# Performance work log

Hardware: AMD Instinct MI355X
Metric: run time of the kernel (lower is better)

The kernel has to match this reference:

```python
import jax, jax.numpy as jnp
import numpy as np

D_MODEL = 2048
NUM_HEADS = 16
D_K = D_MODEL // NUM_HEADS
THETA = 10000.0
BATCH, SEQ = 2, 2048


def setup_inputs() -> dict:
    key = jax.random.key(0)
    ks = jax.random.split(key, 5)
    scale = 1.0 / np.sqrt(D_MODEL)
    x = jax.random.normal(ks[0], (BATCH, SEQ, D_MODEL), dtype=jnp.float32)
    token_positions = jnp.broadcast_to(jnp.arange(SEQ, dtype=jnp.int32)[None, :], (BATCH, SEQ))
    Wq = jax.random.normal(ks[1], (D_MODEL, D_MODEL), dtype=jnp.float32) * scale
    Wk = jax.random.normal(ks[2], (D_MODEL, D_MODEL), dtype=jnp.float32) * scale
    Wv = jax.random.normal(ks[3], (D_MODEL, D_MODEL), dtype=jnp.float32) * scale
    Wo = jax.random.normal(ks[4], (D_MODEL, D_MODEL), dtype=jnp.float32) * scale
    return {"x": x, "token_positions": token_positions, "Wq": Wq, "Wk": Wk, "Wv": Wv, "Wo": Wo}


def _apply_rope(t, positions):
    # t: [b, h, s, d_k]; positions: [b, s]. Interleaved-pair rotation.
    half = D_K // 2
    inv_freq = THETA ** (-jnp.arange(0, half, dtype=jnp.float32) * 2.0 / D_K)  # [half]
    ang = positions.astype(jnp.float32)[:, :, None] * inv_freq[None, None, :]  # [b, s, half]
    cos = jnp.cos(ang)[:, None, :, :]  # [b, 1, s, half]
    sin = jnp.sin(ang)[:, None, :, :]
    t2 = t.reshape(*t.shape[:-1], half, 2)
    x1, x2 = t2[..., 0], t2[..., 1]
    r1 = x1 * cos - x2 * sin
    r2 = x1 * sin + x2 * cos
    return jnp.stack([r1, r2], axis=-1).reshape(t.shape)


def reference(x, token_positions, Wq, Wk, Wv, Wo):
    b, s, _ = x.shape
    # Linear layers compute x @ W^T (weight stored as [out, in], no bias)
    def proj(w):
        y = jnp.einsum('bsd,ed->bse', x, w)
        return y.reshape(b, s, NUM_HEADS, D_K).transpose(0, 2, 1, 3)  # b h s d
    Q, K, V = proj(Wq), proj(Wk), proj(Wv)
    Q = _apply_rope(Q, token_positions)
    K = _apply_rope(K, token_positions)
    scores = jnp.einsum('bhqd,bhkd->bhqk', Q, K) / jnp.sqrt(jnp.float32(D_K))
    causal = jnp.tril(jnp.ones((s, s), dtype=bool))
    scores = jnp.where(causal[None, None], scores, jnp.finfo(scores.dtype).min)
    attn = jax.nn.softmax(scores, axis=-1)
    out = jnp.einsum('bhqk,bhkd->bhqd', attn, V)  # b h s d
    out = out.transpose(0, 2, 1, 3).reshape(b, s, D_MODEL)
    return jnp.einsum('bse,de->bsd', out, Wo)
```

## Files before the change

kernel.cpp:

```cpp
#include <hip/hip_runtime.h>
#include <cstdint>
#include <cstddef>

#define D_MODEL 2048
#define NHEAD 16
#define DK 128
#define SEQ 2048
#define BATCH 2
#define NTOK (BATCH * SEQ)
#define NQB 32

typedef __bf16 bf16;
typedef __bf16 bf16x2 __attribute__((ext_vector_type(2)));
typedef __bf16 bf16x4 __attribute__((ext_vector_type(4)));
typedef __bf16 bf16x8 __attribute__((ext_vector_type(8)));
typedef float f32x4 __attribute__((ext_vector_type(4)));

__device__ __forceinline__ void g2lds16(const void* g, void* l) {
  __builtin_amdgcn_global_load_lds(
      (const __attribute__((address_space(1))) void*)g,
      (__attribute__((address_space(3))) void*)l, 16, 0, 0);
}

__device__ __forceinline__ void cstore(float* p, float v) { *p = v; }
__device__ __forceinline__ void cstore(bf16* p, float v) { *p = (bf16)v; }

#define BAR()                              \
  {                                        \
    asm volatile("" ::: "memory");         \
    __builtin_amdgcn_s_barrier();          \
    asm volatile("" ::: "memory");         \
  }

__global__ void k_conv5(const float* __restrict__ X, const float* __restrict__ W0,
                        const float* __restrict__ W1, const float* __restrict__ W2,
                        const float* __restrict__ W3, bf16* __restrict__ xo,
                        bf16* __restrict__ o0, bf16* __restrict__ o1,
                        bf16* __restrict__ o2, bf16* __restrict__ o3,
                        int nx4, int nw4) {
  const float* in;
  bf16* out;
  int n;
  switch (blockIdx.y) {
    case 0: in = X; out = xo; n = nx4; break;
    case 1: in = W0; out = o0; n = nw4; break;
    case 2: in = W1; out = o1; n = nw4; break;
    case 3: in = W2; out = o2; n = nw4; break;
    default: in = W3; out = o3; n = nw4;
  }
  int i = blockIdx.x * blockDim.x + threadIdx.x;
  if (i >= n) return;
  const float4 v = ((const float4*)in)[i];
  bf16x4 o = {(bf16)v.x, (bf16)v.y, (bf16)v.z, (bf16)v.w};
  ((bf16x4*)out)[i] = o;
}

__global__ __launch_bounds__(512, 1) void k_gemm8(
    const bf16* __restrict__ A, const bf16* __restrict__ B0p, const bf16* __restrict__ B1p,
    const bf16* __restrict__ B2p, bf16* __restrict__ C0, bf16* __restrict__ C1,
    bf16* __restrict__ C2, const int* __restrict__ pos, int M, int N, int K) {
  const bf16* Bp = B0p;
  bf16* Cp = C0;
  if (blockIdx.z == 1) { Bp = B1p; Cp = C1; }
  else if (blockIdx.z == 2) { Bp = B2p; Cp = C2; }
  const bool rope = (blockIdx.z < 2);

  __shared__ bf16 Ab[2][256 * 64];
  __shared__ bf16 Bb[2][256 * 64];

  const int t = threadIdx.x;
  const int wid = t >> 6, lane = t & 63;
  const int wr = wid >> 2, wc = wid & 3;
  const int lr = lane & 15, lg = lane >> 4;
  const int bm = blockIdx.y, bn = blockIdx.x;
  const size_t arow0 = (size_t)bm * 256;
  const size_t brow0 = (size_t)bn * 256;

  const int srow = wid * 8 + (lane >> 3);
  const int schunk = ((lane & 7) ^ ((lane >> 3) & 7)) * 8;

#define STG(X, row0, k0, lb, h)                                                \
  {                                                                            \
    g2lds16(&(X)[((row0) + (h)*128 + srow) * (size_t)K + (k0) + schunk],       \
            &(lb)[((h)*128 + wid * 8) * 64]);                                  \
    g2lds16(&(X)[((row0) + (h)*128 + 64 + srow) * (size_t)K + (k0) + schunk],  \
            &(lb)[((h)*128 + 64 + wid * 8) * 64]);                             \
  }
#define LDA8(lb, mh, m, kk) \
  (*(const bf16x8*)&(lb)[((mh)*128 + wr * 64 + (m)*16 + lr) * 64 + ((((kk)*4 + lg) ^ (lr & 7)) * 8)])
#define LDB8(lb, nh, n, kk) \
  (*(const bf16x8*)&(lb)[((nh)*128 + wc * 32 + (n)*16 + lr) * 64 + ((((kk)*4 + lg) ^ (lr & 7)) * 8)])

  const int T = K >> 6;

  STG(A, arow0, 0, Ab[0], 0);
  STG(A, arow0, 0, Ab[0], 1);
  STG(Bp, brow0, 0, Bb[0], 0);
  STG(Bp, brow0, 0, Bb[0], 1);
  STG(A, arow0, 64, Ab[1], 0);

  f32x4 acc[2][2][4][2] = {};

  for (int tt = 0; tt < T; ++tt) {
    const int cur = tt & 1;
    const bf16* Ac = Ab[cur];
    const bf16* Bc = Bb[cur];
    bf16* Aw = Ab[cur];
    bf16* An = Ab[cur ^ 1];
    bf16* Bn = Bb[cur ^ 1];
    const int k1 = (tt + 1) << 6;
    const int k2 = (tt + 2) << 6;
    const bool pf1 = (tt + 1 < T);
    const bool pf2 = (tt + 2 < T);

    if (tt == T - 1) {
      asm volatile("s_waitcnt vmcnt(0)" ::: "memory");
    } else {
      asm volatile("s_waitcnt vmcnt(2)" ::: "memory");
    }
    BAR();

    bf16x8 a[4][2], b0[2][2], b1[2][2];

#pragma unroll
    for (int m = 0; m < 4; ++m)
#pragma unroll
      for (int kk = 0; kk < 2; ++kk) a[m][kk] = LDA8(Ac, 0, m, kk);
#pragma unroll
    for (int n = 0; n < 2; ++n)
#pragma unroll
      for (int kk = 0; kk < 2; ++kk) b0[n][kk] = LDB8(Bc, 0, n, kk);
    if (pf1) {
      STG(A, arow0, k1, An, 1);
      STG(Bp, brow0, k1, Bn, 0);
    }
    __builtin_amdgcn_s_setprio(1);
#pragma unroll
    for (int m = 0; m < 4; ++m)
#pragma unroll
      for (int n = 0; n < 2; ++n)
#pragma unroll
        for (int kk = 0; kk < 2; ++kk)
          acc[0][0][m][n] =
              __builtin_amdgcn_mfma_f32_16x16x32_bf16(a[m][kk], b0[n][kk], acc[0][0][m][n], 0, 0, 0);
    __builtin_amdgcn_s_setprio(0);
    BAR();

#pragma unroll
    for (int n = 0; n < 2; ++n)
#pragma unroll
      for (int kk = 0; kk < 2; ++kk) b1[n][kk] = LDB8(Bc, 1, n, kk);
    if (pf1) STG(Bp, brow0, k1, Bn, 1);
    __builtin_amdgcn_s_setprio(1);
#pragma unroll
    for (int m = 0; m < 4; ++m)
#pragma unroll
      for (int n = 0; n < 2; ++n)
#pragma unroll
        for (int kk = 0; kk < 2; ++kk)
          acc[0][1][m][n] =
              __builtin_amdgcn_mfma_f32_16x16x32_bf16(a[m][kk], b1[n][kk], acc[0][1][m][n], 0, 0, 0);
    __builtin_amdgcn_s_setprio(0);

#pragma unroll
    for (int m = 0; m < 4; ++m)
#pragma unroll
      for (int kk = 0; kk < 2; ++kk) a[m][kk] = LDA8(Ac, 1, m, kk);
    if (pf2) STG(A, arow0, k2, Aw, 0);
    __builtin_amdgcn_s_setprio(1);
#pragma unroll
    for (int m = 0; m < 4; ++m)
#pragma unroll
      for (int n = 0; n < 2; ++n)
#pragma unroll
        for (int kk = 0; kk < 2; ++kk)
          acc[1][1][m][n] =
              __builtin_amdgcn_mfma_f32_16x16x32_bf16(a[m][kk], b1[n][kk], acc[1][1][m][n], 0, 0, 0);

#pragma unroll
    for (int m = 0; m < 4; ++m)
#pragma unroll
      for (int n = 0; n < 2; ++n)
#pragma unroll
        for (int kk = 0; kk < 2; ++kk)
          acc[1][0][m][n] =
              __builtin_amdgcn_mfma_f32_16x16x32_bf16(a[m][kk], b0[n][kk], acc[1][0][m][n], 0, 0, 0);
    __builtin_amdgcn_s_setprio(0);
  }

  float invf[2];
#pragma unroll
  for (int n = 0; n < 2; ++n) {
    int f = ((wc * 32 + n * 16 + lr) & 127) >> 1;
    invf[n] = exp2f((float)f * -0.20762050593121503f);
  }
#pragma unroll
  for (int mh = 0; mh < 2; ++mh)
#pragma unroll
    for (int m = 0; m < 4; ++m) {
      size_t rowb = arow0 + mh * 128 + wr * 64 + m * 16 + lg * 4;
#pragma unroll
      for (int r = 0; r < 4; ++r) {
        float p = rope ? (float)pos[rowb + r] : 0.0f;
#pragma unroll
        for (int n = 0; n < 2; ++n) {
          float sn, cs;
          if (rope) __sincosf(p * invf[n], &sn, &cs);
#pragma unroll
          for (int nh = 0; nh < 2; ++nh) {
            float v = acc[mh][nh][m][n][r];
            float vp = __shfl_xor(v, 1);
            float outv = v;
            if (rope) outv = (lr & 1) ? (v * cs + vp * sn) : (v * cs - vp * sn);
            size_t col = brow0 + nh * 128 + wc * 32 + n * 16 + lr;
            Cp[(rowb + r) * N + col] = (bf16)outv;
          }
        }
      }
    }
#undef STG
#undef LDA8
#undef LDB8
}

__global__ __launch_bounds__(512, 1) void k_gemmPV(
    const bf16* __restrict__ A, const bf16* __restrict__ Bp, bf16* __restrict__ Cp,
    int M, int N, int K) {
  const int wg = blockIdx.x;
  const int bn = wg & 7;
  const int bm = wg >> 3;

  __shared__ bf16 Ab[2][128 * 64];
  __shared__ bf16 Bb[2][256 * 64];

  const int t = threadIdx.x;
  const int wid = t >> 6, lane = t & 63;
  const int wr = wid >> 2, wc = wid & 3;
  const int lr = lane & 15, lg = lane >> 4;
  const size_t arow0 = (size_t)bm * 128;
  const size_t brow0 = (size_t)bn * 256;

  const int srow = wid * 8 + (lane >> 3);
  const int schunk = ((lane & 7) ^ ((lane >> 3) & 7)) * 8;

#define STGA(X, k0, lb, h) \
  g2lds16(&(X)[(arow0 + (h)*64 + srow) * (size_t)K + (k0) + schunk], &(lb)[((h)*64 + wid * 8) * 64]);
#define STGB(X, k0, lb, h)                                                        \
  {                                                                               \
    g2lds16(&(X)[(brow0 + (h)*128 + srow) * (size_t)K + (k0) + schunk],           \
            &(lb)[((h)*128 + wid * 8) * 64]);                                     \
    g2lds16(&(X)[(brow0 + (h)*128 + 64 + srow) * (size_t)K + (k0) + schunk],      \
            &(lb)[((h)*128 + 64 + wid * 8) * 64]);                                \
  }
#define LDA8(lb, mh, m, kk) \
  (*(const bf16x8*)&(lb)[((mh)*64 + wr * 32 + (m)*16 + lr) * 64 + ((((kk)*4 + lg) ^ (lr & 7)) * 8)])
#define LDB8(lb, nh, n, kk) \
  (*(const bf16x8*)&(lb)[((nh)*128 + wc * 32 + (n)*16 + lr) * 64 + ((((kk)*4 + lg) ^ (lr & 7)) * 8)])

  const int T = K >> 6;

  STGA(A, 0, Ab[0], 0);
  STGA(A, 0, Ab[0], 1);
  STGB(Bp, 0, Bb[0], 0);
  STGB(Bp, 0, Bb[0], 1);
  STGA(A, 64, Ab[1], 0);

  f32x4 acc[2][2][2][2] = {};

  for (int tt = 0; tt < T; ++tt) {
    const int cur = tt & 1;
    const bf16* Ac = Ab[cur];
    const bf16* Bc = Bb[cur];
    bf16* Aw = Ab[cur];
    bf16* An = Ab[cur ^ 1];
    bf16* Bn = Bb[cur ^ 1];
    const int k1 = (tt + 1) << 6;
    const int k2 = (tt + 2) << 6;
    const bool pf1 = (tt + 1 < T);
    const bool pf2 = (tt + 2 < T);

    if (tt == T - 1) {
      asm volatile("s_waitcnt vmcnt(0)" ::: "memory");
    } else {
      asm volatile("s_waitcnt vmcnt(1)" ::: "memory");
    }
    BAR();

    bf16x8 a[2][2], b[2][2];

#pragma unroll
    for (int m = 0; m < 2; ++m)
#pragma unroll
      for (int kk = 0; kk < 2; ++kk) a[m][kk] = LDA8(Ac, 0, m, kk);
#pragma unroll
    for (int n = 0; n < 2; ++n)
#pragma unroll
      for (int kk = 0; kk < 2; ++kk) b[n][kk] = LDB8(Bc, 0, n, kk);
    if (pf1) {
      STGA(A, k1, An, 1);
      STGB(Bp, k1, Bn, 0);
    }
    __builtin_amdgcn_s_setprio(1);
#pragma unroll
    for (int m = 0; m < 2; ++m)
#pragma unroll
      for (int n = 0; n < 2; ++n)
#pragma unroll
        for (int kk = 0; kk < 2; ++kk)
          acc[0][0][m][n] =
              __builtin_amdgcn_mfma_f32_16x16x32_bf16(a[m][kk], b[n][kk], acc[0][0][m][n], 0, 0, 0);
    __builtin_amdgcn_s_setprio(0);
    BAR();

#pragma unroll
    for (int n = 0; n < 2; ++n)
#pragma unroll
      for (int kk = 0; kk < 2; ++kk) b[n][kk] = LDB8(Bc, 1, n, kk);
    if (pf1) STGB(Bp, k1, Bn, 1);
    __builtin_amdgcn_s_setprio(1);
#pragma unroll
    for (int m = 0; m < 2; ++m)
#pragma unroll
      for (int n = 0; n < 2; ++n)
#pragma unroll
        for (int kk = 0; kk < 2; ++kk)
          acc[0][1][m][n] =
              __builtin_amdgcn_mfma_f32_16x16x32_bf16(a[m][kk], b[n][kk], acc[0][1][m][n], 0, 0, 0);
    __builtin_amdgcn_s_setprio(0);
    BAR();

#pragma unroll
    for (int m = 0; m < 2; ++m)
#pragma unroll
      for (int kk = 0; kk < 2; ++kk) a[m][kk] = LDA8(Ac, 1, m, kk);
    if (pf2) STGA(A, k2, Aw, 0);
    __builtin_amdgcn_s_setprio(1);
#pragma unroll
    for (int m = 0; m < 2; ++m)
#pragma unroll
      for (int n = 0; n < 2; ++n)
#pragma unroll
        for (int kk = 0; kk < 2; ++kk)
          acc[1][1][m][n] =
              __builtin_amdgcn_mfma_f32_16x16x32_bf16(a[m][kk], b[n][kk], acc[1][1][m][n], 0, 0, 0);
    __builtin_amdgcn_s_setprio(0);
    BAR();

#pragma unroll
    for (int n = 0; n < 2; ++n)
#pragma unroll
      for (int kk = 0; kk < 2; ++kk) b[n][kk] = LDB8(Bc, 0, n, kk);
    __builtin_amdgcn_s_setprio(1);
#pragma unroll
    for (int m = 0; m < 2; ++m)
#pragma unroll
      for (int n = 0; n < 2; ++n)
#pragma unroll
        for (int kk = 0; kk < 2; ++kk)
          acc[1][0][m][n] =
              __builtin_amdgcn_mfma_f32_16x16x32_bf16(a[m][kk], b[n][kk], acc[1][0][m][n], 0, 0, 0);
    __builtin_amdgcn_s_setprio(0);
  }

#pragma unroll
  for (int mh = 0; mh < 2; ++mh)
#pragma unroll
    for (int nh = 0; nh < 2; ++nh)
#pragma unroll
      for (int m = 0; m < 2; ++m) {
        size_t rowb = arow0 + mh * 64 + wr * 32 + m * 16 + lg * 4;
#pragma unroll
        for (int n = 0; n < 2; ++n) {
          size_t col = brow0 + nh * 128 + wc * 32 + n * 16 + lr;
#pragma unroll
          for (int r = 0; r < 4; ++r) Cp[(rowb + r) * N + col] = (bf16)acc[mh][nh][m][n][r];
        }
      }
#undef STGA
#undef STGB
#undef LDA8
#undef LDB8
}

__global__ __launch_bounds__(256, 4) void k_vtrans(const bf16* __restrict__ V,
                                                   bf16* __restrict__ VT) {
  const int bh = blockIdx.z;
  const int b = bh >> 4, h = bh & 15;
  const int tt64 = blockIdx.x * 64;
  const int t = threadIdx.x;
  __shared__ bf16 L[128][72];
  const int tok_l = t & 63, dc0 = t >> 6;
#pragma unroll
  for (int p = 0; p < 4; ++p) {
    int dc = dc0 * 4 + p;
    bf16x8 v = *(const bf16x8*)&V[((size_t)(b * SEQ) + tt64 + tok_l) * D_MODEL + h * DK + dc * 8];
#pragma unroll
    for (int j = 0; j < 8; ++j) L[dc * 8 + j][tok_l] = v[j];
  }
  __syncthreads();
  const int d = t >> 1, half = t & 1;
  const size_t obase = ((size_t)bh * DK + d) * SEQ + tt64;
#pragma unroll
  for (int i = 0; i < 4; ++i) {
    int g = half * 4 + i;
    *(bf16x8*)&VT[obase + g * 8] = *(const bf16x8*)&L[d][g * 8];
  }
}

template <typename OutT>
__global__ __launch_bounds__(256, 2) void k_gemm_nt(
    const bf16* __restrict__ A, const bf16* __restrict__ B0, const bf16* __restrict__ B1,
    const bf16* __restrict__ B2, OutT* __restrict__ C0, OutT* __restrict__ C1,
    OutT* __restrict__ C2, int M, int N, int K) {
  const bf16* Bp = B0;
  OutT* Cp = C0;
  if (blockIdx.z == 1) { Bp = B1; Cp = C1; }
  else if (blockIdx.z == 2) { Bp = B2; Cp = C2; }

  __shared__ bf16 As[128 * 32];
  __shared__ bf16 Bs[128 * 32];

  const int t = threadIdx.x;
  const int w = t >> 6;
  const int lane = t & 63;
  const int lr = lane & 15;
  const int lg = lane >> 4;
  const int wr = w >> 1, wc = w & 1;
  const int bm = blockIdx.y, bn = blockIdx.x;

  f32x4 acc[4][4] = {};

  const int srow = lane >> 2;
  const int scol = (lane & 3) * 8;

  const int kt_iters = K >> 5;
  for (int kt = 0; kt < kt_iters; ++kt) {
    const int kbase = kt * 32;
#pragma unroll
    for (int i = 0; i < 2; ++i) {
      int chunk = w * 2 + i;
      int row = chunk * 16 + srow;
      g2lds16(&A[(size_t)(bm * 128 + row) * K + kbase + scol], &As[chunk * 512]);
      g2lds16(&Bp[(size_t)(bn * 128 + row) * K + kbase + scol], &Bs[chunk * 512]);
    }
    asm volatile("s_waitcnt vmcnt(0)" ::: "memory");
    __syncthreads();

    bf16x8 af[4], bfr[4];
#pragma unroll
    for (int m = 0; m < 4; ++m)
      af[m] = *(const bf16x8*)&As[(wr * 64 + m * 16 + lr) * 32 + lg * 8];
#pragma unroll
    for (int n = 0; n < 4; ++n)
      bfr[n] = *(const bf16x8*)&Bs[(wc * 64 + n * 16 + lr) * 32 + lg * 8];
#pragma unroll
    for (int m = 0; m < 4; ++m)
#pragma unroll
      for (int n = 0; n < 4; ++n)
        acc[m][n] = __builtin_amdgcn_mfma_f32_16x16x32_bf16(af[m], bfr[n], acc[m][n], 0, 0, 0);
    __syncthreads();
  }

#pragma unroll
  for (int m = 0; m < 4; ++m) {
    int rowb = bm * 128 + wr * 64 + m * 16 + lg * 4;
#pragma unroll
    for (int n = 0; n < 4; ++n) {
      int col = bn * 128 + wc * 64 + n * 16 + lr;
#pragma unroll
      for (int r = 0; r < 4; ++r) cstore(&Cp[(size_t)(rowb + r) * N + col], acc[m][n][r]);
    }
  }
}

__global__ __launch_bounds__(256, 2) void k_attn(const bf16* __restrict__ Q,
                                                 const bf16* __restrict__ K,
                                                 const bf16* __restrict__ VT,
                                                 bf16* __restrict__ O) {
  const int wg = blockIdx.x;
  const int g = wg & 7;
  const int i = wg >> 3;
  const int bh = g + 8 * (i & 3);
  const int pr = i >> 2;
  const int b = bh >> 4, h = bh & 15;

  const int t = threadIdx.x;
  const int w = t >> 6, lane = t & 63;
  const int lr = lane & 15, lg = lane >> 4;

  const size_t rowbase = (size_t)b * SEQ;
  const int hoff = h * DK;
  const size_t vtbase = (size_t)bh * DK * SEQ;

  __shared__ bf16 Ks[2][64 * 128];
  __shared__ bf16 VTb[2][128 * 64];
  __shared__ bf16 Pb[4][16 * 64];

  const float scale = 0.08838834764831845f;
  const float FIXM = 8.0f;

  int cur = 0;

  const int krow_l = lane >> 4;
  const int kchunk = lane & 15;
  const int vrow_l = lane >> 3;
  const int vchunk = lane & 7;

#define STGK(k0v, buf)                                                         \
  _Pragma("unroll") for (int j_ = 0; j_ < 4; ++j_) {                           \
    int row_ = w * 16 + j_ * 4 + krow_l;                                       \
    int ck_ = kchunk ^ (row_ & 15);                                            \
    g2lds16(&K[(rowbase + (k0v) + row_) * D_MODEL + hoff + ck_ * 8],           \
            &Ks[buf][(size_t)(w * 16 + j_ * 4) * 128]);                        \
  }
#define STGV(k0v, buf)                                                         \
  _Pragma("unroll") for (int j_ = 0; j_ < 4; ++j_) {                           \
    int d_ = w * 32 + j_ * 8 + vrow_l;                                         \
    int ck_ = vchunk ^ (d_ & 7);                                               \
    g2lds16(&VT[vtbase + (size_t)d_ * SEQ + (k0v) + ck_ * 8],                  \
            &VTb[buf][(size_t)(w * 32 + j_ * 8) * 64]);                        \
  }

  for (int qsel = 0; qsel < 2; ++qsel) {
    const int qblk = qsel ? pr : (NQB - 1 - pr);
    const int qb = qblk * 64;
    const int ktiles = qblk + 1;

    bf16x8 qf[4];
    {
      size_t qrow = rowbase + qb + w * 16 + lr;
#pragma unroll
      for (int c = 0; c < 4; ++c)
        qf[c] = *(const bf16x8*)&Q[qrow * D_MODEL + hoff + c * 32 + lg * 8];
    }

    f32x4 o[8] = {};
    f32x4 lrow = {};

    STGK(0, cur);
    STGV(0, cur);

    for (int kt = 0; kt < ktiles; ++kt) {
      const int k0 = kt * 64;
      asm volatile("s_waitcnt vmcnt(0)" ::: "memory");
      __syncthreads();

      if (kt + 1 < ktiles) {
        STGK(k0 + 64, cur ^ 1);
        STGV(k0 + 64, cur ^ 1);
      }

      f32x4 sc[4];
      __builtin_amdgcn_s_setprio(1);
#pragma unroll
      for (int tt = 0; tt < 4; ++tt) {
        f32x4 a = {};
#pragma unroll
        for (int c = 0; c < 4; ++c) {
          bf16x8 kf = *(const bf16x8*)&Ks[cur][(tt * 16 + lr) * 128 + (((c * 4 + lg) ^ lr) * 8)];
          a = __builtin_amdgcn_mfma_f32_16x16x32_bf16(qf[c], kf, a, 0, 0, 0);
        }
        sc[tt] = a * scale;
      }
      __builtin_amdgcn_s_setprio(0);

      const int qrow0 = qb + w * 16 + lg * 4;
      if (k0 + 64 > qb + w * 16) {
#pragma unroll
        for (int tt = 0; tt < 4; ++tt) {
          int kcol = k0 + tt * 16 + lr;
#pragma unroll
          for (int r = 0; r < 4; ++r)
            if (kcol > qrow0 + r) sc[tt][r] = -3.0e38f;
        }
      }

#pragma unroll
      for (int tt = 0; tt < 4; ++tt)
#pragma unroll
        for (int r = 0; r < 4; ++r) {
          float p = __expf(sc[tt][r] - FIXM);
          sc[tt][r] = p;
          lrow[r] += p;
        }

#pragma unroll
      for (int tt = 0; tt < 4; ++tt)
#pragma unroll
        for (int r = 0; r < 4; ++r) {
          int q = lg * 4 + r;
          int col = tt * 16 + lr;
          Pb[w][q * 64 + (col ^ ((q & 7) << 3))] = (bf16)sc[tt][r];
        }
      asm volatile("s_waitcnt lgkmcnt(0)" ::: "memory");
      bf16x8 pf0 = *(const bf16x8*)&Pb[w][lr * 64 + ((lg * 8) ^ ((lr & 7) << 3))];
      bf16x8 pf1 = *(const bf16x8*)&Pb[w][lr * 64 + ((32 + lg * 8) ^ ((lr & 7) << 3))];

      __builtin_amdgcn_s_setprio(1);
#pragma unroll
      for (int nt = 0; nt < 8; ++nt) {
        int d = nt * 16 + lr;
        bf16x8 vf0 = *(const bf16x8*)&VTb[cur][d * 64 + ((lg ^ (d & 7)) * 8)];
        bf16x8 vf1 = *(const bf16x8*)&VTb[cur][d * 64 + (((4 + lg) ^ (d & 7)) * 8)];
        o[nt] = __builtin_amdgcn_mfma_f32_16x16x32_bf16(pf0, vf0, o[nt], 0, 0, 0);
        o[nt] = __builtin_amdgcn_mfma_f32_16x16x32_bf16(pf1, vf1, o[nt], 0, 0, 0);
      }
      __builtin_amdgcn_s_setprio(0);
      cur ^= 1;
    }

#pragma unroll
    for (int off = 8; off >= 1; off >>= 1)
#pragma unroll
      for (int r = 0; r < 4; ++r) lrow[r] += __shfl_xor(lrow[r], off);

    size_t orow = rowbase + qb + w * 16 + lg * 4;
#pragma unroll
    for (int nt = 0; nt < 8; ++nt)
#pragma unroll
      for (int r = 0; r < 4; ++r)
        O[(orow + r) * D_MODEL + hoff + nt * 16 + lr] = (bf16)(o[nt][r] / lrow[r]);
  }
#undef STGK
#undef STGV
}

extern "C" void kernel_launch(void* const* d_in, const int* in_sizes, int n_in, void* d_out,
                              int out_size, void* d_ws, size_t ws_size, hipStream_t stream) {
  const float* x = (const float*)d_in[0];
  const int* pos = (const int*)d_in[1];
  const float* Wq = (const float*)d_in[2];
  const float* Wk = (const float*)d_in[3];
  const float* Wv = (const float*)d_in[4];
  const float* Wo = (const float*)d_in[5];
  float* out = (float*)d_out;

  char* ws = (char*)d_ws;
  const size_t MB = 1u << 20;
  bf16* xb  = (bf16*)(ws);
  bf16* wqb = (bf16*)(ws + 16 * MB);
  bf16* wkb = (bf16*)(ws + 24 * MB);
  bf16* wvb = (bf16*)(ws + 32 * MB);
  bf16* wob = (bf16*)(ws + 40 * MB);
  bf16* Qb  = (bf16*)(ws + 48 * MB);
  bf16* Kb  = (bf16*)(ws + 64 * MB);
  bf16* Vb  = (bf16*)(ws + 80 * MB);
  bf16* AOb = (bf16*)(ws + 96 * MB);
  bf16* VTg = xb;

  {
    int nx4 = NTOK * D_MODEL / 4;
    int nw4 = D_MODEL * D_MODEL / 4;
    k_conv5<<<dim3((nx4 + 255) / 256, 5), 256, 0, stream>>>(
        x, Wq, Wk, Wv, Wo, xb, wqb, wkb, wvb, wob, nx4, nw4);
  }
  {
    dim3 g(D_MODEL / 256, NTOK / 256, 2);
    k_gemm8<<<g, 512, 0, stream>>>(xb, wqb, wkb, wkb, Qb, Kb, Kb, pos,
                                   NTOK, D_MODEL, D_MODEL);
  }
  k_gemmPV<<<256, 512, 0, stream>>>(xb, wvb, Vb, NTOK, D_MODEL, D_MODEL);
  k_vtrans<<<dim3(SEQ / 64, 1, BATCH * NHEAD), 256, 0, stream>>>(Vb, VTg);
  k_attn<<<dim3(NQB * NHEAD * BATCH / 2, 1, 1), 256, 0, stream>>>(Qb, Kb, VTg, AOb);
  {
    dim3 g(D_MODEL / 128, NTOK / 128, 1);
    k_gemm_nt<float><<<g, 256, 0, stream>>>(AOb, wob, wob, wob, out, out, out, NTOK, D_MODEL, D_MODEL);
  }
}
```

Baseline: 262.7 us.

## Compute V transposed directly via swapped GEMM operands, drop transpose kernel

The V projection is now computed as Wv·xᵀ per batch (operands swapped, grid y over batch), so the GEMM writes Vᵀ in the [b,h,d,seq] layout the attention kernel reads. This removes the separate transpose kernel and its extra global-memory round trip. The attention kernel also folds log2(e) into the score scale and fixed max so it can use the native exp2 instruction. K/V staging addresses are precomputed once and advanced by pointer increments instead of being recomputed each tile. The swapped GEMM has a smaller M per launch (2048 per batch), which may change tile utilisation.

```diff
diff --git a/kernel.cpp b/kernel.cpp
--- a/kernel.cpp
+++ b/kernel.cpp
@@ -224,11 +224,14 @@
 }
 
 __global__ __launch_bounds__(512, 1) void k_gemmPV(
-    const bf16* __restrict__ A, const bf16* __restrict__ Bp, bf16* __restrict__ Cp,
+    const bf16* __restrict__ A, const bf16* __restrict__ Bx, bf16* __restrict__ Cv,
     int M, int N, int K) {
   const int wg = blockIdx.x;
   const int bn = wg & 7;
   const int bm = wg >> 3;
+  const size_t boff = (size_t)blockIdx.y * 2048 * 2048;
+  const bf16* Bp = Bx + boff;
+  bf16* Cp = Cv + boff;
 
   __shared__ bf16 Ab[2][128 * 64];
   __shared__ bf16 Bb[2][256 * 64];
@@ -382,31 +385,6 @@
 #undef LDB8
 }
 
-__global__ __launch_bounds__(256, 4) void k_vtrans(const bf16* __restrict__ V,
-                                                   bf16* __restrict__ VT) {
-  const int bh = blockIdx.z;
-  const int b = bh >> 4, h = bh & 15;
-  const int tt64 = blockIdx.x * 64;
-  const int t = threadIdx.x;
-  __shared__ bf16 L[128][72];
-  const int tok_l = t & 63, dc0 = t >> 6;
-#pragma unroll
-  for (int p = 0; p < 4; ++p) {
-    int dc = dc0 * 4 + p;
-    bf16x8 v = *(const bf16x8*)&V[((size_t)(b * SEQ) + tt64 + tok_l) * D_MODEL + h * DK + dc * 8];
-#pragma unroll
-    for (int j = 0; j < 8; ++j) L[dc * 8 + j][tok_l] = v[j];
-  }
-  __syncthreads();
-  const int d = t >> 1, half = t & 1;
-  const size_t obase = ((size_t)bh * DK + d) * SEQ + tt64;
-#pragma unroll
-  for (int i = 0; i < 4; ++i) {
-    int g = half * 4 + i;
-    *(bf16x8*)&VT[obase + g * 8] = *(const bf16x8*)&L[d][g * 8];
-  }
-}
-
 template <typename OutT>
 __global__ __launch_bounds__(256, 2) void k_gemm_nt(
     const bf16* __restrict__ A, const bf16* __restrict__ B0, const bf16* __restrict__ B1,
@@ -496,8 +474,8 @@
   __shared__ bf16 VTb[2][128 * 64];
   __shared__ bf16 Pb[4][16 * 64];
 
-  const float scale = 0.08838834764831845f;
-  const float FIXM = 8.0f;
+  const float scale2 = 0.12751744672f;
+  const float FIXM2 = 11.5415603271f;
 
   int cur = 0;
 
@@ -506,21 +484,6 @@
   const int vrow_l = lane >> 3;
   const int vchunk = lane & 7;
 
-#define STGK(k0v, buf)                                                         \
-  _Pragma("unroll") for (int j_ = 0; j_ < 4; ++j_) {                           \
-    int row_ = w * 16 + j_ * 4 + krow_l;                                       \
-    int ck_ = kchunk ^ (row_ & 15);                                            \
-    g2lds16(&K[(rowbase + (k0v) + row_) * D_MODEL + hoff + ck_ * 8],           \
-            &Ks[buf][(size_t)(w * 16 + j_ * 4) * 128]);                        \
-  }
-#define STGV(k0v, buf)                                                         \
-  _Pragma("unroll") for (int j_ = 0; j_ < 4; ++j_) {                           \
-    int d_ = w * 32 + j_ * 8 + vrow_l;                                         \
-    int ck_ = vchunk ^ (d_ & 7);                                               \
-    g2lds16(&VT[vtbase + (size_t)d_ * SEQ + (k0v) + ck_ * 8],                  \
-            &VTb[buf][(size_t)(w * 32 + j_ * 8) * 64]);                        \
-  }
-
   for (int qsel = 0; qsel < 2; ++qsel) {
     const int qblk = qsel ? pr : (NQB - 1 - pr);
     const int qb = qblk * 64;
@@ -537,8 +500,26 @@
     f32x4 o[8] = {};
     f32x4 lrow = {};
 
-    STGK(0, cur);
-    STGV(0, cur);
+    const bf16* kst[4];
+    const bf16* vst[4];
+#pragma unroll
+    for (int j = 0; j < 4; ++j) {
+      int row_ = w * 16 + j * 4 + krow_l;
+      kst[j] = &K[(rowbase + row_) * D_MODEL + hoff + (kchunk ^ (row_ & 15)) * 8];
+      int d_ = w * 32 + j * 8 + vrow_l;
+      vst[j] = &VT[vtbase + (size_t)d_ * SEQ + (vchunk ^ (d_ & 7)) * 8];
+    }
+
+#pragma unroll
+    for (int j = 0; j < 4; ++j) {
+      g2lds16(kst[j], &Ks[cur][(size_t)(w * 16 + j * 4) * 128]);
+      kst[j] += 64 * D_MODEL;
+    }
+#pragma unroll
+    for (int j = 0; j < 4; ++j) {
+      g2lds16(vst[j], &VTb[cur][(size_t)(w * 32 + j * 8) * 64]);
+      vst[j] += 64;
+    }
 
     for (int kt = 0; kt < ktiles; ++kt) {
       const int k0 = kt * 64;
@@ -546,8 +527,16 @@
       __syncthreads();
 
       if (kt + 1 < ktiles) {
-        STGK(k0 + 64, cur ^ 1);
-        STGV(k0 + 64, cur ^ 1);
+#pragma unroll
+        for (int j = 0; j < 4; ++j) {
+          g2lds16(kst[j], &Ks[cur ^ 1][(size_t)(w * 16 + j * 4) * 128]);
+          kst[j] += 64 * D_MODEL;
+        }
+#pragma unroll
+        for (int j = 0; j < 4; ++j) {
+          g2lds16(vst[j], &VTb[cur ^ 1][(size_t)(w * 32 + j * 8) * 64]);
+          vst[j] += 64;
+        }
       }
 
       f32x4 sc[4];
@@ -560,7 +549,7 @@
           bf16x8 kf = *(const bf16x8*)&Ks[cur][(tt * 16 + lr) * 128 + (((c * 4 + lg) ^ lr) * 8)];
           a = __builtin_amdgcn_mfma_f32_16x16x32_bf16(qf[c], kf, a, 0, 0, 0);
         }
-        sc[tt] = a * scale;
+        sc[tt] = a * scale2;
       }
       __builtin_amdgcn_s_setprio(0);
 
@@ -579,7 +568,7 @@
       for (int tt = 0; tt < 4; ++tt)
 #pragma unroll
         for (int r = 0; r < 4; ++r) {
-          float p = __expf(sc[tt][r] - FIXM);
+          float p = __builtin_amdgcn_exp2f(sc[tt][r] - FIXM2);
           sc[tt][r] = p;
           lrow[r] += p;
         }
@@ -621,8 +610,6 @@
       for (int r = 0; r < 4; ++r)
         O[(orow + r) * D_MODEL + hoff + nt * 16 + lr] = (bf16)(o[nt][r] / lrow[r]);
   }
-#undef STGK
-#undef STGV
 }
 
 extern "C" void kernel_launch(void* const* d_in, const int* in_sizes, int n_in, void* d_out,
@@ -644,9 +631,8 @@
   bf16* wob = (bf16*)(ws + 40 * MB);
   bf16* Qb  = (bf16*)(ws + 48 * MB);
   bf16* Kb  = (bf16*)(ws + 64 * MB);
-  bf16* Vb  = (bf16*)(ws + 80 * MB);
+  bf16* VTg = (bf16*)(ws + 80 * MB);
   bf16* AOb = (bf16*)(ws + 96 * MB);
-  bf16* VTg = xb;
 
   {
     int nx4 = NTOK * D_MODEL / 4;
@@ -659,8 +645,7 @@
     k_gemm8<<<g, 512, 0, stream>>>(xb, wqb, wkb, wkb, Qb, Kb, Kb, pos,
                                    NTOK, D_MODEL, D_MODEL);
   }
-  k_gemmPV<<<256, 512, 0, stream>>>(xb, wvb, Vb, NTOK, D_MODEL, D_MODEL);
-  k_vtrans<<<dim3(SEQ / 64, 1, BATCH * NHEAD), 256, 0, stream>>>(Vb, VTg);
+  k_gemmPV<<<dim3(128, 2), 512, 0, stream>>>(wvb, xb, VTg, D_MODEL, SEQ, D_MODEL);
   k_attn<<<dim3(NQB * NHEAD * BATCH / 2, 1, 1), 256, 0, stream>>>(Qb, Kb, VTg, AOb);
   {
     dim3 g(D_MODEL / 128, NTOK / 128, 1);
```

Result: faster. 244.9 us (median of 2 runs) (-6.8%).
